# Optimization experiments

Hardware: AMD Instinct MI355X
Metric: run time of the kernel (lower is better)

Reference implementation:

```python
import jax, jax.numpy as jnp
import numpy as np

D_MODEL = 256; D_FF = 512; D_STATE = 16; D_CONV = 4; EXPAND = 2
D_INNER = EXPAND * D_MODEL          # 512
DT_RANK = (D_MODEL + 15) // 16      # 16
BSZ = 16; NVARS = 32; PATCH_NUM = 64


def setup_inputs() -> dict:
    key = jax.random.key(0)
    ks = jax.random.split(key, 16)
    def nrm(k, shape, scale=0.02):
        return jax.random.normal(k, shape, jnp.float32) * scale
    inp = {}
    inp["x"] = jax.random.normal(ks[0], (BSZ, NVARS, D_MODEL, PATCH_NUM), jnp.float32)
    # Mamba block params
    inp["in_proj_w"] = nrm(ks[1], (2 * D_INNER, D_MODEL))
    inp["in_proj_b"] = jnp.zeros((2 * D_INNER,), jnp.float32)
    inp["conv_w"] = nrm(ks[2], (D_INNER, D_CONV), 0.1)   # depthwise causal conv
    inp["conv_b"] = jnp.zeros((D_INNER,), jnp.float32)
    inp["x_proj_w"] = nrm(ks[3], (DT_RANK + 2 * D_STATE, D_INNER))
    inp["dt_proj_w"] = nrm(ks[4], (D_INNER, DT_RANK))
    inp["dt_proj_b"] = nrm(ks[5], (D_INNER,), 0.1)
    inp["A_log"] = jnp.log(jnp.broadcast_to(
        jnp.arange(1, D_STATE + 1, dtype=jnp.float32), (D_INNER, D_STATE)))
    inp["Dp"] = jnp.ones((D_INNER,), jnp.float32)
    inp["out_proj_w"] = nrm(ks[6], (D_MODEL, D_INNER))
    # Mamba_ffn norms + pointwise FFN
    inp["norm1_g"] = jnp.ones((D_MODEL,), jnp.float32)
    inp["norm1_b"] = jnp.zeros((D_MODEL,), jnp.float32)
    inp["ffn1_w"] = nrm(ks[7], (D_FF, D_MODEL))
    inp["ffn1_b"] = jnp.zeros((D_FF,), jnp.float32)
    inp["ffn2_w"] = nrm(ks[8], (D_MODEL, D_FF))
    inp["ffn2_b"] = jnp.zeros((D_MODEL,), jnp.float32)
    inp["norm2_g"] = jnp.ones((D_MODEL,), jnp.float32)
    inp["norm2_b"] = jnp.zeros((D_MODEL,), jnp.float32)
    # outer VarPatch LayerNorm
    inp["ln_g"] = jnp.ones((D_MODEL,), jnp.float32)
    inp["ln_b"] = jnp.zeros((D_MODEL,), jnp.float32)
    return inp


def layer_norm(x, g, b, eps=1e-5):
    mu = x.mean(-1, keepdims=True)
    var = ((x - mu) ** 2).mean(-1, keepdims=True)
    return (x - mu) * jax.lax.rsqrt(var + eps) * g + b


def mamba(x, in_proj_w, in_proj_b, conv_w, conv_b, x_proj_w,
          dt_proj_w, dt_proj_b, A_log, Dp, out_proj_w):
    # x: (b, L, d_model)
    b, L, _ = x.shape
    xz = x @ in_proj_w.T + in_proj_b            # (b, L, 2*d_inner)
    xi, z = jnp.split(xz, 2, axis=-1)           # each (b, L, d_inner)
    # causal depthwise conv along L
    xc = xi.transpose(0, 2, 1)                  # (b, d_inner, L)
    xc = jax.lax.conv_general_dilated(
        xc, conv_w[:, None, :], (1,), [(D_CONV - 1, 0)],
        dimension_numbers=("NCH", "OIH", "NCH"),
        feature_group_count=D_INNER) + conv_b[None, :, None]
    xi = jax.nn.silu(xc.transpose(0, 2, 1))     # (b, L, d_inner)
    x_dbl = xi @ x_proj_w.T                     # (b, L, dt_rank + 2*n)
    dt = x_dbl[..., :DT_RANK]
    B = x_dbl[..., DT_RANK:DT_RANK + D_STATE]
    C = x_dbl[..., DT_RANK + D_STATE:]
    delta = jax.nn.softplus(dt @ dt_proj_w.T + dt_proj_b)   # (b, L, d_inner)
    A = -jnp.exp(A_log)                         # (d_inner, n)

    def step(h, inp):
        d_t, B_t, C_t, u_t = inp                # (b,d),(b,n),(b,n),(b,d)
        dA = jnp.exp(d_t[..., None] * A)        # (b, d, n)
        h = dA * h + (d_t * u_t)[..., None] * B_t[:, None, :]
        y = jnp.einsum("bdn,bn->bd", h, C_t)
        return h, y

    h0 = jnp.zeros((b, D_INNER, D_STATE), xi.dtype)
    xs = (delta.transpose(1, 0, 2), B.transpose(1, 0, 2),
          C.transpose(1, 0, 2), xi.transpose(1, 0, 2))
    _, ys = jax.lax.scan(step, h0, xs)          # ys: (L, b, d_inner)
    y = ys.transpose(1, 0, 2) + xi * Dp
    y = y * jax.nn.silu(z)
    return y @ out_proj_w.T                     # (b, L, d_model)


def reference(x, in_proj_w, in_proj_b, conv_w, conv_b, x_proj_w,
              dt_proj_w, dt_proj_b, A_log, Dp, out_proj_w,
              norm1_g, norm1_b, ffn1_w, ffn1_b, ffn2_w, ffn2_b,
              norm2_g, norm2_b, ln_g, ln_b):
    b, nv, dm, pn = x.shape
    x_residual = x
    h = x.reshape(b, pn * nv, dm)               # same flat view as torch reshape
    # Mamba_ffn: mamba + residual, norm, pointwise FFN + residual, norm
    h = h + mamba(h, in_proj_w, in_proj_b, conv_w, conv_b, x_proj_w,
                  dt_proj_w, dt_proj_b, A_log, Dp, out_proj_w)
    h = layer_norm(h, norm1_g, norm1_b)
    y = jax.nn.relu(h @ ffn1_w.T + ffn1_b)      # 1x1 conv == linear
    y = y @ ffn2_w.T + ffn2_b
    h = layer_norm(h + y, norm2_g, norm2_b)
    # back to patches
    h = h.reshape(b, nv, pn, dm)
    h = layer_norm(h, ln_g, ln_b).transpose(0, 1, 3, 2)   # (b, nv, dm, pn)
    return h + x_residual
```

## Files before the change

kernel.cpp:

```cpp
#include <hip/hip_runtime.h>
#include <hip/hip_bf16.h>
#include <math.h>

#define SEQ    2048
#define NBTOT  16
#define NCH    64
#define CHL    32

#define L2E 1.4426950408889634f

typedef __attribute__((ext_vector_type(8))) __bf16 bf16x8;
typedef __attribute__((ext_vector_type(4))) float f32x4;
typedef __attribute__((ext_vector_type(2))) float f32x2;

#define GLOAD16(gp, lp)                                                   \
  __builtin_amdgcn_global_load_lds(                                       \
      (const __attribute__((address_space(1))) unsigned int*)(gp),        \
      (__attribute__((address_space(3))) unsigned int*)(lp), 16, 0, 0)

__device__ __forceinline__ float exp2_(float x) {
  return __builtin_amdgcn_exp2f(x);
}
__device__ __forceinline__ float silu_(float x) {
  return x * __builtin_amdgcn_rcpf(1.f + exp2_(-x * L2E));
}
__device__ __forceinline__ float softplus_(float x) {
  return fmaxf(x, 0.f) + __logf(1.f + exp2_(-fabsf(x) * L2E));
}
__device__ __forceinline__ float wsum_(float v) {
#pragma unroll
  for (int off = 32; off > 0; off >>= 1) v += __shfl_xor(v, off, 64);
  return v;
}
__device__ __forceinline__ void powpairs_(float e1, f32x2 p[8]) {
  float e2 = e1 * e1;
  f32x2 p0; p0.x = e1; p0.y = e2;
  f32x2 s2; s2.x = e2; s2.y = e2;
  f32x2 s4 = s2 * s2;
  f32x2 s8 = s4 * s4;
  p[0] = p0;      p[1] = p0 * s2; p[2] = p0 * s4; p[3] = p[1] * s4;
  p[4] = p0 * s8; p[5] = p[1] * s8; p[6] = p[2] * s8; p[7] = p[3] * s8;
}

template <bool BIAS, bool RELU, bool RES, bool RESB, bool F32OUT, bool BF16OUT>
__global__ __launch_bounds__(256) void gemm_bf16(
    const __hip_bfloat16* __restrict__ A, const __hip_bfloat16* __restrict__ W,
    const float* __restrict__ bias, const float* __restrict__ res,
    const __hip_bfloat16* __restrict__ resb, float* __restrict__ C,
    __hip_bfloat16* __restrict__ Cb, int N, int K) {
  __shared__ __align__(16) short Als[128 * 64];
  __shared__ __align__(16) short Bls[128 * 64];
  const int tid = threadIdx.x;
  const int lane = tid & 63;
  const int wid = tid >> 6;
  const int m0 = blockIdx.y * 128;
  const int n0 = blockIdx.x * 128;
  const int wm = (wid >> 1) * 64;
  const int wn = (wid & 1) * 64;
  const int lr = lane & 15;
  const int lk = lane >> 4;

  f32x4 acc[4][4];
#pragma unroll
  for (int m = 0; m < 4; ++m)
#pragma unroll
    for (int n = 0; n < 4; ++n) acc[m][n] = (f32x4){0.f, 0.f, 0.f, 0.f};

  const int srow = wid * 32 + (lane >> 3);
  const int scol = (lane & 7) * 8;
  const __hip_bfloat16* Ag = A + (size_t)(m0 + srow) * K + scol;
  const __hip_bfloat16* Wg = W + (size_t)(n0 + srow) * K + scol;
  short* Alb = Als + wid * 2048;
  short* Blb = Bls + wid * 2048;

  for (int kt = 0; kt < K; kt += 64) {
#pragma unroll
    for (int i = 0; i < 4; ++i) {
      GLOAD16(Ag + (size_t)(i * 8) * K + kt, Alb + i * 512);
      GLOAD16(Wg + (size_t)(i * 8) * K + kt, Blb + i * 512);
    }
    __syncthreads();
    const bf16x8* Af = reinterpret_cast<const bf16x8*>(Als);
    const bf16x8* Bf = reinterpret_cast<const bf16x8*>(Bls);
#pragma unroll
    for (int ks = 0; ks < 2; ++ks) {
      bf16x8 av[4], bv[4];
#pragma unroll
      for (int m = 0; m < 4; ++m)
        av[m] = Af[(wm + m * 16 + lr) * 8 + ks * 4 + lk];
#pragma unroll
      for (int n = 0; n < 4; ++n)
        bv[n] = Bf[(wn + n * 16 + lr) * 8 + ks * 4 + lk];
#pragma unroll
      for (int m = 0; m < 4; ++m)
#pragma unroll
        for (int n = 0; n < 4; ++n)
          acc[m][n] = __builtin_amdgcn_mfma_f32_16x16x32_bf16(
              av[m], bv[n], acc[m][n], 0, 0, 0);
    }
    __syncthreads();
  }

#pragma unroll
  for (int n = 0; n < 4; ++n) {
    int col = n0 + wn + n * 16 + lr;
    if (col >= N) continue;
    float bval = BIAS ? bias[col] : 0.f;
#pragma unroll
    for (int m = 0; m < 4; ++m) {
      int row0 = m0 + wm + m * 16 + lk * 4;
#pragma unroll
      for (int r = 0; r < 4; ++r) {
        size_t off = (size_t)(row0 + r) * N + col;
        float v = acc[m][n][r];
        if (BIAS) v += bval;
        if (RES) v += res[off];
        if (RESB) v += __bfloat162float(resb[off]);
        if (RELU) v = fmaxf(v, 0.f);
        if (F32OUT) C[off] = v;
        if (BF16OUT) Cb[off] = __float2bfloat16(v);
      }
    }
  }
}

__global__ __launch_bounds__(256) void cast_bf16_k(
    const float* __restrict__ src, __hip_bfloat16* __restrict__ dst, int n4) {
  int i = blockIdx.x * 256 + threadIdx.x;
  if (i >= n4) return;
  float4 v = reinterpret_cast<const float4*>(src)[i];
  union { __hip_bfloat16 h[4]; short4 s4; } u;
  u.h[0] = __float2bfloat16(v.x); u.h[1] = __float2bfloat16(v.y);
  u.h[2] = __float2bfloat16(v.z); u.h[3] = __float2bfloat16(v.w);
  reinterpret_cast<short4*>(dst)[i] = u.s4;
}

__global__ __launch_bounds__(256) void pad_wx_k(
    const float* __restrict__ src, __hip_bfloat16* __restrict__ dst) {
  int i = blockIdx.x * 256 + threadIdx.x;
  int row = i >> 7;
  union { __hip_bfloat16 h[4]; short4 s4; } u;
  if (row < 48) {
    float4 v = reinterpret_cast<const float4*>(src)[i];
    u.h[0] = __float2bfloat16(v.x); u.h[1] = __float2bfloat16(v.y);
    u.h[2] = __float2bfloat16(v.z); u.h[3] = __float2bfloat16(v.w);
  } else {
    u.h[0] = u.h[1] = u.h[2] = u.h[3] = __float2bfloat16(0.f);
  }
  reinterpret_cast<short4*>(dst)[i] = u.s4;
}

__global__ __launch_bounds__(256) void conv_silu_k(
    const __hip_bfloat16* __restrict__ xz, const float* __restrict__ cw,
    const float* __restrict__ cb, __hip_bfloat16* __restrict__ xi) {
  int idx = blockIdx.x * 256 + threadIdx.x;
  int t = idx & 63;
  int r = idx >> 6;
  int l = r & (SEQ - 1);
  int c8 = t << 3;
  const __hip_bfloat16* p = xz + (size_t)r * 1024 + c8;
  union U8 { int4 v; __hip_bfloat16 h[8]; } x0, x1, x2, x3, o;
  const int4 z4 = make_int4(0, 0, 0, 0);
  x3.v = *reinterpret_cast<const int4*>(p);
  x2.v = (l >= 1) ? *reinterpret_cast<const int4*>(p - 1024) : z4;
  x1.v = (l >= 2) ? *reinterpret_cast<const int4*>(p - 2048) : z4;
  x0.v = (l >= 3) ? *reinterpret_cast<const int4*>(p - 3072) : z4;
  const float4* cw4 = reinterpret_cast<const float4*>(cw);
#pragma unroll
  for (int j = 0; j < 8; ++j) {
    float4 w = cw4[c8 + j];
    float acc = cb[c8 + j];
    acc = fmaf(w.x, __bfloat162float(x0.h[j]), acc);
    acc = fmaf(w.y, __bfloat162float(x1.h[j]), acc);
    acc = fmaf(w.z, __bfloat162float(x2.h[j]), acc);
    acc = fmaf(w.w, __bfloat162float(x3.h[j]), acc);
    o.h[j] = __float2bfloat16(silu_(acc));
  }
  reinterpret_cast<int4*>(xi)[idx] = o.v;
}

__global__ __launch_bounds__(256) void scan_p1(
    const __hip_bfloat16* __restrict__ u, const float* __restrict__ xdbl,
    const float* __restrict__ A_log, const float* __restrict__ wdt,
    const float* __restrict__ bdt, float* __restrict__ dlsum,
    __hip_bfloat16* __restrict__ hp, __hip_bfloat16* __restrict__ deltab) {
  const int d = ((blockIdx.x & 1) << 8) + threadIdx.x;
  const int c = blockIdx.x >> 1;
  const int b = blockIdx.y;
  const int l0 = c * CHL;
  float A2[16];
  f32x2 w2[8];
  {
    const float4* aq = reinterpret_cast<const float4*>(&A_log[d * 16]);
    const f32x2* wq = reinterpret_cast<const f32x2*>(&wdt[d * 16]);
#pragma unroll
    for (int q = 0; q < 4; ++q) {
      float4 v = aq[q];
      A2[q * 4 + 0] = -exp2_(v.x * L2E) * L2E;
      A2[q * 4 + 1] = -exp2_(v.y * L2E) * L2E;
      A2[q * 4 + 2] = -exp2_(v.z * L2E) * L2E;
      A2[q * 4 + 3] = -exp2_(v.w * L2E) * L2E;
    }
#pragma unroll
    for (int k = 0; k < 8; ++k) w2[k] = wq[k];
  }
  bool chainok = true;
#pragma unroll
  for (int n = 1; n < 16; ++n)
    chainok = chainok &&
              (fabsf(A2[n] - (float)(n + 1) * A2[0]) <=
               1e-4f * (float)(n + 1) * fabsf(A2[0]));
  const float bdtd = bdt[d];
  const float nL = A2[0];
  f32x2 h2[8];
#pragma unroll
  for (int k = 0; k < 8; ++k) h2[k] = (f32x2){0.f, 0.f};
  float dls = 0.f;
  size_t base = (size_t)(b * SEQ + l0) * 512 + d;
  const float* rowp = xdbl + (size_t)(b * SEQ + l0) * 48;
  if (chainok) {
#pragma unroll 4
    for (int i = 0; i < CHL; ++i) {
      const f32x2* r2 = reinterpret_cast<const f32x2*>(rowp + i * 48);
      f32x2 acc2; acc2.x = bdtd; acc2.y = 0.f;
#pragma unroll
      for (int k = 0; k < 8; ++k)
        acc2 = __builtin_elementwise_fma(r2[k], w2[k], acc2);
      float dl = softplus_(acc2.x + acc2.y);
      deltab[base + (size_t)i * 512] = __float2bfloat16(dl);
      dls += dl;
      float du = dl * __bfloat162float(u[base + (size_t)i * 512]);
      f32x2 p[8];
      powpairs_(exp2_(dl * nL), p);
      f32x2 du2; du2.x = du; du2.y = du;
#pragma unroll
      for (int k = 0; k < 8; ++k)
        h2[k] = __builtin_elementwise_fma(p[k], h2[k], du2 * r2[8 + k]);
    }
  } else {
#pragma unroll 2
    for (int i = 0; i < CHL; ++i) {
      const f32x2* r2 = reinterpret_cast<const f32x2*>(rowp + i * 48);
      f32x2 acc2; acc2.x = bdtd; acc2.y = 0.f;
#pragma unroll
      for (int k = 0; k < 8; ++k)
        acc2 = __builtin_elementwise_fma(r2[k], w2[k], acc2);
      float dl = softplus_(acc2.x + acc2.y);
      deltab[base + (size_t)i * 512] = __float2bfloat16(dl);
      dls += dl;
      float du = dl * __bfloat162float(u[base + (size_t)i * 512]);
      f32x2 du2; du2.x = du; du2.y = du;
#pragma unroll
      for (int k = 0; k < 8; ++k) {
        f32x2 a; a.x = exp2_(dl * A2[2 * k]); a.y = exp2_(dl * A2[2 * k + 1]);
        h2[k] = __builtin_elementwise_fma(a, h2[k], du2 * r2[8 + k]);
      }
    }
  }
  size_t sc = (size_t)(b * NCH + c) * 512 + d;
  dlsum[sc] = dls;
  union { __hip_bfloat16 h[4]; short4 s4; } o0, o1, o2, o3;
#pragma unroll
  for (int j = 0; j < 2; ++j) {
    o0.h[2*j] = __float2bfloat16(h2[j].x);   o0.h[2*j+1] = __float2bfloat16(h2[j].y);
    o1.h[2*j] = __float2bfloat16(h2[2+j].x); o1.h[2*j+1] = __float2bfloat16(h2[2+j].y);
    o2.h[2*j] = __float2bfloat16(h2[4+j].x); o2.h[2*j+1] = __float2bfloat16(h2[4+j].y);
    o3.h[2*j] = __float2bfloat16(h2[6+j].x); o3.h[2*j+1] = __float2bfloat16(h2[6+j].y);
  }
  short4* hq = reinterpret_cast<short4*>(hp + sc * 16);
  hq[0] = o0.s4; hq[1] = o1.s4; hq[2] = o2.s4; hq[3] = o3.s4;
}

__global__ __launch_bounds__(256) void scan_p2(
    __hip_bfloat16* hp, const float* __restrict__ dlsum,
    const float* __restrict__ A_log) {
  int g = blockIdx.x * 256 + threadIdx.x;
  int b = g >> 13;
  int dn = g & 8191;
  int d = dn >> 4;
  float A2n = -exp2_(A_log[dn] * L2E) * L2E;
  float H = 0.f;
  for (int c = 0; c < NCH; ++c) {
    float ds = dlsum[(size_t)(b * NCH + c) * 512 + d];
    size_t idx = (size_t)(b * NCH + c) * 8192 + dn;
    float p = __bfloat162float(hp[idx]);
    float a = exp2_(A2n * ds);
    hp[idx] = __float2bfloat16(H);
    H = fmaf(a, H, p);
  }
}

__global__ __launch_bounds__(256) void scan_p3(
    const __hip_bfloat16* u,
    const float* __restrict__ A_log,
    const __hip_bfloat16* __restrict__ deltab, const float* __restrict__ xdbl,
    const __hip_bfloat16* __restrict__ Hc, const float* __restrict__ Dp,
    const __hip_bfloat16* __restrict__ xz, __hip_bfloat16* y) {
  const int d = ((blockIdx.x & 1) << 8) + threadIdx.x;
  const int c = blockIdx.x >> 1;
  const int b = blockIdx.y;
  const int l0 = c * CHL;
  float A2[16];
  {
    const float4* aq = reinterpret_cast<const float4*>(&A_log[d * 16]);
#pragma unroll
    for (int q = 0; q < 4; ++q) {
      float4 v = aq[q];
      A2[q * 4 + 0] = -exp2_(v.x * L2E) * L2E;
      A2[q * 4 + 1] = -exp2_(v.y * L2E) * L2E;
      A2[q * 4 + 2] = -exp2_(v.z * L2E) * L2E;
      A2[q * 4 + 3] = -exp2_(v.w * L2E) * L2E;
    }
  }
  bool chainok = true;
#pragma unroll
  for (int n = 1; n < 16; ++n)
    chainok = chainok &&
              (fabsf(A2[n] - (float)(n + 1) * A2[0]) <=
               1e-4f * (float)(n + 1) * fabsf(A2[0]));
  const float nL = A2[0];
  f32x2 h2[8];
  {
    const short4* hq =
        reinterpret_cast<const short4*>(Hc + ((size_t)(b * NCH + c) * 512 + d) * 16);
#pragma unroll
    for (int q = 0; q < 4; ++q) {
      union { short4 s4; __hip_bfloat16 h[4]; } iv;
      iv.s4 = hq[q];
      h2[2*q].x = __bfloat162float(iv.h[0]);
      h2[2*q].y = __bfloat162float(iv.h[1]);
      h2[2*q+1].x = __bfloat162float(iv.h[2]);
      h2[2*q+1].y = __bfloat162float(iv.h[3]);
    }
  }
  const float Dpd = Dp[d];
  size_t base = (size_t)(b * SEQ + l0) * 512 + d;
  const float* rowp = xdbl + (size_t)(b * SEQ + l0) * 48;
  const __hip_bfloat16* zp = xz + (size_t)(b * SEQ + l0) * 1024 + 512 + d;
  if (chainok) {
#pragma unroll 4
    for (int i = 0; i < CHL; ++i) {
      const f32x2* r2 = reinterpret_cast<const f32x2*>(rowp + i * 48);
      float dl = __bfloat162float(deltab[base + (size_t)i * 512]);
      float ul = __bfloat162float(u[base + (size_t)i * 512]);
      float du = dl * ul;
      f32x2 p[8];
      powpairs_(exp2_(dl * nL), p);
      f32x2 du2; du2.x = du; du2.y = du;
      f32x2 yv2; yv2.x = 0.f; yv2.y = 0.f;
#pragma unroll
      for (int k = 0; k < 8; ++k) {
        h2[k] = __builtin_elementwise_fma(p[k], h2[k], du2 * r2[8 + k]);
        yv2 = __builtin_elementwise_fma(h2[k], r2[16 + k], yv2);
      }
      float yv = yv2.x + yv2.y;
      float zv = __bfloat162float(zp[(size_t)i * 1024]);
      y[base + (size_t)i * 512] =
          __float2bfloat16((yv + ul * Dpd) * silu_(zv));
    }
  } else {
#pragma unroll 2
    for (int i = 0; i < CHL; ++i) {
      const f32x2* r2 = reinterpret_cast<const f32x2*>(rowp + i * 48);
      float dl = __bfloat162float(deltab[base + (size_t)i * 512]);
      float ul = __bfloat162float(u[base + (size_t)i * 512]);
      float du = dl * ul;
      f32x2 du2; du2.x = du; du2.y = du;
      f32x2 yv2; yv2.x = 0.f; yv2.y = 0.f;
#pragma unroll
      for (int k = 0; k < 8; ++k) {
        f32x2 a; a.x = exp2_(dl * A2[2 * k]); a.y = exp2_(dl * A2[2 * k + 1]);
        h2[k] = __builtin_elementwise_fma(a, h2[k], du2 * r2[8 + k]);
        yv2 = __builtin_elementwise_fma(h2[k], r2[16 + k], yv2);
      }
      float yv = yv2.x + yv2.y;
      float zv = __bfloat162float(zp[(size_t)i * 1024]);
      y[base + (size_t)i * 512] =
          __float2bfloat16((yv + ul * Dpd) * silu_(zv));
    }
  }
}

__global__ __launch_bounds__(256) void ln_k(
    const __hip_bfloat16* __restrict__ in, const float* __restrict__ g,
    const float* __restrict__ bb, __hip_bfloat16* __restrict__ outb) {
  int row = (blockIdx.x * 256 + threadIdx.x) >> 6;
  int lane = threadIdx.x & 63;
  union { short4 s4; __hip_bfloat16 h[4]; } iv;
  iv.s4 = reinterpret_cast<const short4*>(in)[row * 64 + lane];
  float v0 = __bfloat162float(iv.h[0]), v1 = __bfloat162float(iv.h[1]);
  float v2 = __bfloat162float(iv.h[2]), v3 = __bfloat162float(iv.h[3]);
  float mu = wsum_(v0 + v1 + v2 + v3) * (1.f / 256.f);
  float a0 = v0 - mu, a1 = v1 - mu, a2 = v2 - mu, a3 = v3 - mu;
  float var = wsum_(a0 * a0 + a1 * a1 + a2 * a2 + a3 * a3) * (1.f / 256.f);
  float rs = __builtin_amdgcn_rsqf(var + 1e-5f);
  float4 gg = *reinterpret_cast<const float4*>(&g[lane * 4]);
  float4 bq = *reinterpret_cast<const float4*>(&bb[lane * 4]);
  union { __hip_bfloat16 h[4]; short4 s4; } u;
  u.h[0] = __float2bfloat16(a0 * rs * gg.x + bq.x);
  u.h[1] = __float2bfloat16(a1 * rs * gg.y + bq.y);
  u.h[2] = __float2bfloat16(a2 * rs * gg.z + bq.z);
  u.h[3] = __float2bfloat16(a3 * rs * gg.w + bq.w);
  reinterpret_cast<short4*>(outb)[row * 64 + lane] = u.s4;
}

__global__ __launch_bounds__(256) void final_k(
    const __hip_bfloat16* __restrict__ t2, const float* __restrict__ g2v,
    const float* __restrict__ b2v, const float* __restrict__ g3v,
    const float* __restrict__ b3v, const float* __restrict__ x,
    float* __restrict__ out) {
  int bx = blockIdx.x;
  int half = bx & 1, nv = (bx >> 1) & 31, b = bx >> 6;
  int wave = threadIdx.x >> 6, lane = threadIdx.x & 63;
  __shared__ float sh[32][257];
  float4 gg2 = *reinterpret_cast<const float4*>(&g2v[lane * 4]);
  float4 bb2 = *reinterpret_cast<const float4*>(&b2v[lane * 4]);
  float4 gg3 = *reinterpret_cast<const float4*>(&g3v[lane * 4]);
  float4 bb3 = *reinterpret_cast<const float4*>(&b3v[lane * 4]);
#pragma unroll
  for (int i = 0; i < 8; ++i) {
    int pn = wave * 8 + i;
    int r = ((b * 32 + nv) << 6) + (half << 5) + pn;
    union { short4 s4; __hip_bfloat16 h[4]; } iv;
    iv.s4 = reinterpret_cast<const short4*>(t2)[r * 64 + lane];
    float v0 = __bfloat162float(iv.h[0]), v1 = __bfloat162float(iv.h[1]);
    float v2 = __bfloat162float(iv.h[2]), v3 = __bfloat162float(iv.h[3]);
    float mu = wsum_(v0 + v1 + v2 + v3) * (1.f / 256.f);
    float a0 = v0 - mu, a1 = v1 - mu, a2 = v2 - mu, a3 = v3 - mu;
    float var = wsum_(a0 * a0 + a1 * a1 + a2 * a2 + a3 * a3) * (1.f / 256.f);
    float rs = __builtin_amdgcn_rsqf(var + 1e-5f);
    a0 = a0 * rs * gg2.x + bb2.x; a1 = a1 * rs * gg2.y + bb2.y;
    a2 = a2 * rs * gg2.z + bb2.z; a3 = a3 * rs * gg2.w + bb2.w;
    mu = wsum_(a0 + a1 + a2 + a3) * (1.f / 256.f);
    float c0 = a0 - mu, c1 = a1 - mu, c2 = a2 - mu, c3 = a3 - mu;
    var = wsum_(c0 * c0 + c1 * c1 + c2 * c2 + c3 * c3) * (1.f / 256.f);
    rs = __builtin_amdgcn_rsqf(var + 1e-5f);
    sh[pn][lane * 4 + 0] = c0 * rs * gg3.x + bb3.x;
    sh[pn][lane * 4 + 1] = c1 * rs * gg3.y + bb3.y;
    sh[pn][lane * 4 + 2] = c2 * rs * gg3.z + bb3.z;
    sh[pn][lane * 4 + 3] = c3 * rs * gg3.w + bb3.w;
  }
  __syncthreads();
  int pnl = threadIdx.x & 31;
  int dbase = threadIdx.x >> 5;
  size_t obase = (size_t)((b * 32 + nv) * 256) * 64 + (half << 5) + pnl;
#pragma unroll
  for (int k = 0; k < 32; ++k) {
    int dd = dbase + (k << 3);
    size_t oi = obase + (size_t)dd * 64;
    out[oi] = sh[pnl][dd] + x[oi];
  }
}

extern "C" void kernel_launch(void* const* d_in, const int* in_sizes, int n_in,
                              void* d_out, int out_size, void* d_ws,
                              size_t ws_size, hipStream_t stream) {
  const float* x    = (const float*)d_in[0];
  const float* w_in = (const float*)d_in[1];
  const float* b_in = (const float*)d_in[2];
  const float* cw   = (const float*)d_in[3];
  const float* cb   = (const float*)d_in[4];
  const float* wx   = (const float*)d_in[5];
  const float* wdt  = (const float*)d_in[6];
  const float* bdt  = (const float*)d_in[7];
  const float* alog = (const float*)d_in[8];
  const float* Dp   = (const float*)d_in[9];
  const float* wout = (const float*)d_in[10];
  const float* g1   = (const float*)d_in[11];
  const float* b1   = (const float*)d_in[12];
  const float* wf1  = (const float*)d_in[13];
  const float* bf1  = (const float*)d_in[14];
  const float* wf2  = (const float*)d_in[15];
  const float* bf2  = (const float*)d_in[16];
  const float* g2   = (const float*)d_in[17];
  const float* b2   = (const float*)d_in[18];
  const float* g3   = (const float*)d_in[19];
  const float* b3   = (const float*)d_in[20];
  float* out = (float*)d_out;

  const size_t MB1 = 1048576;
  char* g = (char*)d_ws;
  __hip_bfloat16* wbf_in  = (__hip_bfloat16*)(g);
  __hip_bfloat16* wbf_out = (__hip_bfloat16*)(g + 524288);
  __hip_bfloat16* wbf_f1  = (__hip_bfloat16*)(g + 786432);
  __hip_bfloat16* wbf_f2  = (__hip_bfloat16*)(g + 1048576);
  __hip_bfloat16* wbf_xp  = (__hip_bfloat16*)(g + 1310720);
  const size_t SHARED = 1572864;

  const size_t PB = 11 * MB1 + 393216;
  int nb = (int)((ws_size - SHARED) / PB);
  if (ws_size <= SHARED || nb < 1) return;
  if (nb > NBTOT) nb = NBTOT;

  dim3 blk(256);
  cast_bf16_k<<<dim3(256), blk, 0, stream>>>(w_in, wbf_in, 65536);
  cast_bf16_k<<<dim3(128), blk, 0, stream>>>(wout, wbf_out, 32768);
  cast_bf16_k<<<dim3(128), blk, 0, stream>>>(wf1, wbf_f1, 32768);
  cast_bf16_k<<<dim3(128), blk, 0, stream>>>(wf2, wbf_f2, 32768);
  pad_wx_k<<<dim3(64), blk, 0, stream>>>(wx, wbf_xp);

  for (int b0 = 0; b0 < NBTOT; b0 += nb) {
    int bn = (NBTOT - b0 < nb) ? (NBTOT - b0) : nb;
    char* base = g + SHARED;
    char* RA = base;
    char* RB = base + (size_t)bn * 4 * MB1;
    char* RC = base + (size_t)bn * 5 * MB1;
    char* RD = base + (size_t)bn * 7 * MB1;
    char* RE = RD + (size_t)bn * 393216;
    char* RF = RE + (size_t)bn * 2 * MB1;

    __hip_bfloat16* xz     = (__hip_bfloat16*)RA;
    __hip_bfloat16* t2b    = (__hip_bfloat16*)RA;
    __hip_bfloat16* xbf    = (__hip_bfloat16*)RB;
    float*          dlsum  = (float*)RB;
    __hip_bfloat16* xibf   = (__hip_bfloat16*)RC;
    __hip_bfloat16* ffnybf = (__hip_bfloat16*)RC;
    float*          xdbl   = (float*)RD;
    __hip_bfloat16* hp     = (__hip_bfloat16*)RE;
    __hip_bfloat16* resb   = (__hip_bfloat16*)RE;
    __hip_bfloat16* h1bf   = (__hip_bfloat16*)(RE + (size_t)bn * MB1);
    __hip_bfloat16* deltab = (__hip_bfloat16*)RF;

    const float* xg = x + (size_t)b0 * SEQ * 256;
    float* outg = out + (size_t)b0 * SEQ * 256;
    int M = bn * SEQ;
    int MT = M / 128;

    cast_bf16_k<<<dim3(M * 64 / 256), blk, 0, stream>>>(xg, xbf, M * 64);
    gemm_bf16<true, false, false, false, false, true>
        <<<dim3(8, MT), blk, 0, stream>>>(xbf, wbf_in, b_in, nullptr, nullptr,
                                          nullptr, xz, 1024, 256);
    conv_silu_k<<<dim3(M / 4), blk, 0, stream>>>(xz, cw, cb, xibf);
    gemm_bf16<false, false, false, false, true, false>
        <<<dim3(1, MT), blk, 0, stream>>>(xibf, wbf_xp, nullptr, nullptr,
                                          nullptr, xdbl, nullptr, 48, 512);
    scan_p1<<<dim3(NCH * 2, bn), blk, 0, stream>>>(xibf, xdbl, alog, wdt, bdt,
                                                   dlsum, hp, deltab);
    scan_p2<<<dim3(bn * 32), blk, 0, stream>>>(hp, dlsum, alog);
    scan_p3<<<dim3(NCH * 2, bn), blk, 0, stream>>>(xibf, alog, deltab, xdbl,
                                                   hp, Dp, xz, xibf);
    gemm_bf16<false, false, true, false, false, true>
        <<<dim3(2, MT), blk, 0, stream>>>(xibf, wbf_out, nullptr, xg, nullptr,
                                          nullptr, resb, 256, 512);
    ln_k<<<dim3(M / 4), blk, 0, stream>>>(resb, g1, b1, h1bf);
    gemm_bf16<true, true, false, false, false, true>
        <<<dim3(4, MT), blk, 0, stream>>>(h1bf, wbf_f1, bf1, nullptr, nullptr,
                                          nullptr, ffnybf, 512, 256);
    gemm_bf16<true, false, false, true, false, true>
        <<<dim3(2, MT), blk, 0, stream>>>(ffnybf, wbf_f2, bf2, nullptr, h1bf,
                                          nullptr, t2b, 256, 512);
    final_k<<<dim3(bn * 64), blk, 0, stream>>>(t2b, g2, b2, g3, b3, xg, outg);
  }
}
```

Measured before the change: 303.1 us.

## Stage bf16 GEMM epilogue through LDS and swizzle block order across XCDs

The bf16-output GEMM epilogue now writes each wave's tile to a padded shared-memory buffer and stores it to global memory as 16-byte row-contiguous vectors, replacing scattered 2-byte column stores. The grid is flattened to 1D and block indices are remapped so consecutive tiles land on the same XCD with contiguous M/N ranges, aiming for better L2 reuse. Shared memory grows to 36 KB, which may lower occupancy, and the bf16 path drops the column bound check, assuming N is a multiple of 128.

```diff
diff --git a/kernel.cpp b/kernel.cpp
--- a/kernel.cpp
+++ b/kernel.cpp
@@ -42,19 +42,23 @@
   p[4] = p0 * s8; p[5] = p[1] * s8; p[6] = p[2] * s8; p[7] = p[3] * s8;
 }
 
-template <bool BIAS, bool RELU, bool RES, bool RESB, bool F32OUT, bool BF16OUT>
+template <bool BIAS, bool RELU, bool RES, bool RESB, bool F32OUT, bool BF16OUT,
+          int NTLOG>
 __global__ __launch_bounds__(256) void gemm_bf16(
     const __hip_bfloat16* __restrict__ A, const __hip_bfloat16* __restrict__ W,
     const float* __restrict__ bias, const float* __restrict__ res,
     const __hip_bfloat16* __restrict__ resb, float* __restrict__ C,
     __hip_bfloat16* __restrict__ Cb, int N, int K) {
-  __shared__ __align__(16) short Als[128 * 64];
-  __shared__ __align__(16) short Bls[128 * 64];
+  __shared__ __align__(16) char ShRaw[36864];
+  short* Als = reinterpret_cast<short*>(ShRaw);
+  short* Bls = Als + 8192;
   const int tid = threadIdx.x;
   const int lane = tid & 63;
   const int wid = tid >> 6;
-  const int m0 = blockIdx.y * 128;
-  const int n0 = blockIdx.x * 128;
+  const int nwg = gridDim.x;
+  const int swz = (blockIdx.x & 7) * (nwg >> 3) + (blockIdx.x >> 3);
+  const int m0 = (swz >> NTLOG) * 128;
+  const int n0 = (swz & ((1 << NTLOG) - 1)) * 128;
   const int wm = (wid >> 1) * 64;
   const int wn = (wid & 1) * 64;
   const int lr = lane & 15;
@@ -101,24 +105,57 @@
     __syncthreads();
   }
 
-#pragma unroll
-  for (int n = 0; n < 4; ++n) {
-    int col = n0 + wn + n * 16 + lr;
-    if (col >= N) continue;
-    float bval = BIAS ? bias[col] : 0.f;
-#pragma unroll
-    for (int m = 0; m < 4; ++m) {
-      int row0 = m0 + wm + m * 16 + lk * 4;
-#pragma unroll
-      for (int r = 0; r < 4; ++r) {
-        size_t off = (size_t)(row0 + r) * N + col;
-        float v = acc[m][n][r];
-        if (BIAS) v += bval;
-        if (RES) v += res[off];
-        if (RESB) v += __bfloat162float(resb[off]);
-        if (RELU) v = fmaxf(v, 0.f);
-        if (F32OUT) C[off] = v;
-        if (BF16OUT) Cb[off] = __float2bfloat16(v);
+  if (BF16OUT) {
+    __hip_bfloat16* epi =
+        reinterpret_cast<__hip_bfloat16*>(ShRaw) + wid * 4608;
+#pragma unroll
+    for (int n = 0; n < 4; ++n) {
+      int col = n0 + wn + n * 16 + lr;
+      float bval = BIAS ? bias[col] : 0.f;
+#pragma unroll
+      for (int m = 0; m < 4; ++m) {
+        int lrow = m * 16 + lk * 4;
+#pragma unroll
+        for (int r = 0; r < 4; ++r) {
+          float v = acc[m][n][r];
+          if (BIAS) v += bval;
+          if (RES) v += res[(size_t)(m0 + wm + lrow + r) * N + col];
+          if (RESB)
+            v += __bfloat162float(resb[(size_t)(m0 + wm + lrow + r) * N + col]);
+          if (RELU) v = fmaxf(v, 0.f);
+          epi[(lrow + r) * 72 + n * 16 + lr] = __float2bfloat16(v);
+        }
+      }
+    }
+    const int lr8 = (lane & 7) * 8;
+    const int lrw = lane >> 3;
+    const size_t obase = (size_t)(m0 + wm) * N + n0 + wn + lr8;
+#pragma unroll
+    for (int j = 0; j < 8; ++j) {
+      int row = j * 8 + lrw;
+      int4 vv = *reinterpret_cast<const int4*>(epi + row * 72 + lr8);
+      *reinterpret_cast<int4*>(&Cb[obase + (size_t)row * N]) = vv;
+    }
+  }
+  if (F32OUT) {
+#pragma unroll
+    for (int n = 0; n < 4; ++n) {
+      int col = n0 + wn + n * 16 + lr;
+      if (col >= N) continue;
+      float bval = BIAS ? bias[col] : 0.f;
+#pragma unroll
+      for (int m = 0; m < 4; ++m) {
+        int row0 = m0 + wm + m * 16 + lk * 4;
+#pragma unroll
+        for (int r = 0; r < 4; ++r) {
+          size_t off = (size_t)(row0 + r) * N + col;
+          float v = acc[m][n][r];
+          if (BIAS) v += bval;
+          if (RES) v += res[off];
+          if (RESB) v += __bfloat162float(resb[off]);
+          if (RELU) v = fmaxf(v, 0.f);
+          C[off] = v;
+        }
       }
     }
   }
@@ -527,28 +564,28 @@
     int MT = M / 128;
 
     cast_bf16_k<<<dim3(M * 64 / 256), blk, 0, stream>>>(xg, xbf, M * 64);
-    gemm_bf16<true, false, false, false, false, true>
-        <<<dim3(8, MT), blk, 0, stream>>>(xbf, wbf_in, b_in, nullptr, nullptr,
-                                          nullptr, xz, 1024, 256);
+    gemm_bf16<true, false, false, false, false, true, 3>
+        <<<dim3(8 * MT), blk, 0, stream>>>(xbf, wbf_in, b_in, nullptr, nullptr,
+                                           nullptr, xz, 1024, 256);
     conv_silu_k<<<dim3(M / 4), blk, 0, stream>>>(xz, cw, cb, xibf);
-    gemm_bf16<false, false, false, false, true, false>
-        <<<dim3(1, MT), blk, 0, stream>>>(xibf, wbf_xp, nullptr, nullptr,
-                                          nullptr, xdbl, nullptr, 48, 512);
+    gemm_bf16<false, false, false, false, true, false, 0>
+        <<<dim3(MT), blk, 0, stream>>>(xibf, wbf_xp, nullptr, nullptr,
+                                       nullptr, xdbl, nullptr, 48, 512);
     scan_p1<<<dim3(NCH * 2, bn), blk, 0, stream>>>(xibf, xdbl, alog, wdt, bdt,
                                                    dlsum, hp, deltab);
     scan_p2<<<dim3(bn * 32), blk, 0, stream>>>(hp, dlsum, alog);
     scan_p3<<<dim3(NCH * 2, bn), blk, 0, stream>>>(xibf, alog, deltab, xdbl,
                                                    hp, Dp, xz, xibf);
-    gemm_bf16<false, false, true, false, false, true>
-        <<<dim3(2, MT), blk, 0, stream>>>(xibf, wbf_out, nullptr, xg, nullptr,
-                                          nullptr, resb, 256, 512);
+    gemm_bf16<false, false, true, false, false, true, 1>
+        <<<dim3(2 * MT), blk, 0, stream>>>(xibf, wbf_out, nullptr, xg, nullptr,
+                                           nullptr, resb, 256, 512);
     ln_k<<<dim3(M / 4), blk, 0, stream>>>(resb, g1, b1, h1bf);
-    gemm_bf16<true, true, false, false, false, true>
-        <<<dim3(4, MT), blk, 0, stream>>>(h1bf, wbf_f1, bf1, nullptr, nullptr,
-                                          nullptr, ffnybf, 512, 256);
-    gemm_bf16<true, false, false, true, false, true>
-        <<<dim3(2, MT), blk, 0, stream>>>(ffnybf, wbf_f2, bf2, nullptr, h1bf,
-                                          nullptr, t2b, 256, 512);
+    gemm_bf16<true, true, false, false, false, true, 2>
+        <<<dim3(4 * MT), blk, 0, stream>>>(h1bf, wbf_f1, bf1, nullptr, nullptr,
+                                           nullptr, ffnybf, 512, 256);
+    gemm_bf16<true, false, false, true, false, true, 1>
+        <<<dim3(2 * MT), blk, 0, stream>>>(ffnybf, wbf_f2, bf2, nullptr, h1bf,
+                                           nullptr, t2b, 256, 512);
     final_k<<<dim3(bn * 64), blk, 0, stream>>>(t2b, g2, b2, g3, b3, xg, outg);
   }
 }
```

Result: faster. 280.1 us (-7.6%).
